# Kernel optimization log

Hardware: AMD Instinct MI355X
Metric: run time of the kernel (lower is better)

Reference implementation:

```python
import jax, jax.numpy as jnp
import numpy as np

B, L, D, HD, DC = 2, 2048, 2048, 64, 2048
NH = D // HD  # 32 heads


def _rms_norm(x, eps):
    return x * jax.lax.rsqrt(jnp.mean(jnp.square(x), axis=-1, keepdims=True) + eps)


def _apply_rope(x, rope):
    # x: [b,h,l,d]; rope: [2,l,d]. x_hat = interleave(-x_odd, x_even)
    x2 = x.reshape(*x.shape[:-1], HD // 2, 2)
    x_hat = jnp.stack([-x2[..., 1], x2[..., 0]], axis=-1).reshape(x.shape)
    return x * rope[0] + x_hat * rope[1]


def setup_inputs() -> dict:
    key = jax.random.key(0)
    ks = jax.random.split(key, 6)
    return {
        "x": jax.random.normal(ks[0], (B, L, D), jnp.float32),
        "condition": jax.random.normal(ks[1], (B, DC), jnp.float32),
        "rope": jax.random.normal(ks[2], (2, L, HD), jnp.float32),
        "w_ada": jax.random.normal(ks[3], (2 * D, DC), jnp.float32) * 0.02,
        "w_qkv": jax.random.normal(ks[4], (3 * D, D), jnp.float32) * 0.02,
        "w_out": jax.random.normal(ks[5], (D, D), jnp.float32) * 0.02,
        "qk_w": jnp.ones((HD,), jnp.float32),
    }


def reference(x, condition, rope, w_ada, w_qkv, w_out, qk_w):
    eps = jnp.finfo(x.dtype).eps
    # AdaRMSNorm
    ss = (condition @ w_ada.T)[:, None, :]          # [b,1,2D]
    shift, scale = jnp.split(ss, 2, axis=-1)
    h = _rms_norm(x, eps) * (1.0 + scale) + shift   # [b,l,D]
    # fused QKV projection: 'b l (n h d)'
    qkv = (h @ w_qkv.T).reshape(B, L, 3, NH, HD)
    qkv = jnp.transpose(qkv, (2, 0, 3, 1, 4))       # [3,b,h,l,d]
    q, k, v = qkv[0], qkv[1], qkv[2]
    # per-head RMSNorm (with affine weight) + RoPE
    q = _apply_rope(_rms_norm(q, eps) * qk_w, rope)
    k = _apply_rope(_rms_norm(k, eps) * qk_w, rope)
    # SDPA
    scores = jnp.einsum('bhqd,bhkd->bhqk', q, k) / jnp.sqrt(jnp.asarray(HD, x.dtype))
    attn = jax.nn.softmax(scores, axis=-1)
    o = jnp.einsum('bhqk,bhkd->bhqd', attn, v)      # [b,h,l,d]
    o = jnp.transpose(o, (0, 2, 1, 3)).reshape(B, L, D)
    return o @ w_out.T
```

## Files before the change

kernel.cpp:

```cpp
#include <hip/hip_runtime.h>


typedef __bf16 bf16x8 __attribute__((ext_vector_type(8)));
typedef float  f32x4  __attribute__((ext_vector_type(4)));
typedef float  f32x16 __attribute__((ext_vector_type(16)));

#define EPS_F32 1.1920929e-07f
#define QSCALE 0.18033688011112042f

#if defined(__has_builtin)
#  if __has_builtin(__builtin_amdgcn_exp2f)
#    define EXP2F(x) __builtin_amdgcn_exp2f(x)
#  else
#    define EXP2F(x) __expf((x) * 0.6931471805599453f)
#  endif
#  if __has_builtin(__builtin_amdgcn_rcpf)
#    define RCPF(x) __builtin_amdgcn_rcpf(x)
#  else
#    define RCPF(x) (1.0f / (x))
#  endif
#else
#  define EXP2F(x) __expf((x) * 0.6931471805599453f)
#  define RCPF(x) (1.0f / (x))
#endif

__device__ __forceinline__ float bf2f(unsigned int u16) {
  union { unsigned int i; float f; } v; v.i = (u16 & 0xffffu) << 16; return v.f;
}
__device__ __forceinline__ unsigned short f2bf(float f) {
  union { float f; unsigned int i; } v; v.f = f;
  unsigned int r = v.i + 0x7fffu + ((v.i >> 16) & 1u);
  return (unsigned short)(r >> 16);
}

__device__ __forceinline__ void gload16(const void* g, void* l) {
  __builtin_amdgcn_global_load_lds(
      (const __attribute__((address_space(1))) unsigned int*)(unsigned long long)g,
      (__attribute__((address_space(3))) unsigned int*)(unsigned int)(unsigned long long)l,
      16, 0, 0);
}

__global__ __launch_bounds__(256) void ada_gemm_kernel(
    const float* __restrict__ cond, const float* __restrict__ w_ada,
    float* __restrict__ ss)
{
  const int lane = threadIdx.x & 63;
  const int gw = blockIdx.x * 4 + (threadIdx.x >> 6);
  const int b = gw >> 12;
  const int j = gw & 4095;
  const float4* wr = (const float4*)(w_ada + j * 2048);
  const float4* cr = (const float4*)(cond + b * 2048);
  float acc = 0.f;
  #pragma unroll
  for (int k4 = 0; k4 < 8; ++k4) {
    float4 w = wr[lane + k4 * 64];
    float4 c = cr[lane + k4 * 64];
    acc += w.x * c.x + w.y * c.y + w.z * c.z + w.w * c.w;
  }
  #pragma unroll
  for (int off = 1; off < 64; off <<= 1) acc += __shfl_xor(acc, off);
  if (lane == 0) ss[b * 4096 + j] = acc;
}

__global__ __launch_bounds__(256) void ada_rms_kernel(
    const float* __restrict__ x, const float* __restrict__ ss,
    unsigned short* __restrict__ H)
{
  const int row = blockIdx.x;
  const int b = row >> 11;
  const int tid = threadIdx.x;
  const int lane = tid & 63, wave = tid >> 6;
  const float* xr = x + (size_t)row * 2048;
  float4 v0 = ((const float4*)xr)[tid * 2];
  float4 v1 = ((const float4*)xr)[tid * 2 + 1];
  float ssq = v0.x*v0.x + v0.y*v0.y + v0.z*v0.z + v0.w*v0.w
            + v1.x*v1.x + v1.y*v1.y + v1.z*v1.z + v1.w*v1.w;
  #pragma unroll
  for (int off = 1; off < 64; off <<= 1) ssq += __shfl_xor(ssq, off);
  __shared__ float red[4];
  if (lane == 0) red[wave] = ssq;
  __syncthreads();
  const float tot = red[0] + red[1] + red[2] + red[3];
  const float r = rsqrtf(tot * (1.f / 2048.f) + EPS_F32);
  const int c0 = tid * 8;
  const float* sh = ss + b * 4096;
  float xv[8] = {v0.x, v0.y, v0.z, v0.w, v1.x, v1.y, v1.z, v1.w};
  unsigned int pk[4];
  #pragma unroll
  for (int p = 0; p < 4; ++p) {
    const int c = c0 + p * 2;
    float h0 = xv[p*2+0] * r * (1.f + sh[2048 + c])     + sh[c];
    float h1 = xv[p*2+1] * r * (1.f + sh[2048 + c + 1]) + sh[c + 1];
    pk[p] = (unsigned int)f2bf(h0) | ((unsigned int)f2bf(h1) << 16);
  }
  *(uint4*)&H[(size_t)row * 2048 + c0] = make_uint4(pk[0], pk[1], pk[2], pk[3]);
}

__global__ __launch_bounds__(256) void cast_kernel(
    const float* __restrict__ src, unsigned short* __restrict__ dst, int n4)
{
  const int i = blockIdx.x * 256 + threadIdx.x;
  if (i >= n4) return;
  float4 v = ((const float4*)src)[i];
  unsigned int p0 = (unsigned int)f2bf(v.x) | ((unsigned int)f2bf(v.y) << 16);
  unsigned int p1 = (unsigned int)f2bf(v.z) | ((unsigned int)f2bf(v.w) << 16);
  *(uint2*)&dst[(size_t)i * 4] = make_uint2(p0, p1);
}

template <int MODE>
__global__ __launch_bounds__(256) void gemm_bt_kernel(
    const unsigned short* __restrict__ A,
    const unsigned short* __restrict__ Bw,
    void* __restrict__ Cv,
    unsigned short* __restrict__ vt,
    int M, int N, int K)
{
  __shared__ unsigned short As[128 * 32];
  __shared__ unsigned short Bs[128 * 32];
  const int tid  = threadIdx.x;
  const int lane = tid & 63;
  const int wave = tid >> 6;
  const int wm = (wave >> 1) * 64;
  const int wn = (wave & 1) * 64;
  const int bm = blockIdx.y * 128;
  const int bn = blockIdx.x * 128;

  f32x4 acc[4][4] = {};

  const int sm = tid >> 2;
  const int sk = (tid & 3) * 8;
  const unsigned short* Ap  = A  + (size_t)(bm + sm) * K + sk;
  const unsigned short* Ap2 = Ap + (size_t)64 * K;
  const unsigned short* Bp  = Bw + (size_t)(bn + sm) * K + sk;
  const unsigned short* Bp2 = Bp + (size_t)64 * K;
  unsigned short* lA  = &As[tid * 8];
  unsigned short* lA2 = &As[tid * 8 + 2048];
  unsigned short* lB  = &Bs[tid * 8];
  unsigned short* lB2 = &Bs[tid * 8 + 2048];

  const int fr = lane & 15;
  const int fk = (lane >> 4) * 8;

  for (int k0 = 0; k0 < K; k0 += 32) {
    __syncthreads();
    gload16(Ap  + k0, lA);
    gload16(Ap2 + k0, lA2);
    gload16(Bp  + k0, lB);
    gload16(Bp2 + k0, lB2);
    __syncthreads();

    bf16x8 af[4], bfr[4];
    #pragma unroll
    for (int i = 0; i < 4; ++i)
      af[i] = *(const bf16x8*)&As[(wm + i * 16 + fr) * 32 + fk];
    #pragma unroll
    for (int j = 0; j < 4; ++j)
      bfr[j] = *(const bf16x8*)&Bs[(wn + j * 16 + fr) * 32 + fk];
    #pragma unroll
    for (int i = 0; i < 4; ++i)
      #pragma unroll
      for (int j = 0; j < 4; ++j)
        acc[i][j] = __builtin_amdgcn_mfma_f32_16x16x32_bf16(af[i], bfr[j], acc[i][j], 0, 0, 0);
  }

  const int cr = (lane >> 4) * 4;
  const int cc = lane & 15;
  if (MODE == 2 && bn >= 4096) {
    #pragma unroll
    for (int i = 0; i < 4; ++i)
      #pragma unroll
      for (int j = 0; j < 4; ++j)
        #pragma unroll
        for (int r = 0; r < 4; ++r) {
          const int m  = bm + wm + i * 16 + cr + r;
          const int dg = bn + wn + j * 16 + cc - 4096;
          const int l  = m & 2047;
          const size_t dst = ((size_t)((m >> 11) * 32 + (dg >> 6)) * 64 + (dg & 63)) * 2048
                           + (l >> 6) * 64 + (l & 15) * 4 + ((l >> 4) & 3);
          vt[dst] = f2bf(acc[i][j][r]);
        }
  } else {
    #pragma unroll
    for (int i = 0; i < 4; ++i)
      #pragma unroll
      for (int j = 0; j < 4; ++j)
        #pragma unroll
        for (int r = 0; r < 4; ++r) {
          const int row = bm + wm + i * 16 + cr + r;
          const int col = bn + wn + j * 16 + cc;
          if (MODE != 0)
            ((unsigned short*)Cv)[(size_t)row * N + col] = f2bf(acc[i][j][r]);
          else
            ((float*)Cv)[(size_t)row * N + col] = acc[i][j][r];
        }
  }
}

__global__ __launch_bounds__(256) void qk_rope_kernel(
    unsigned short* __restrict__ QKV, const float* __restrict__ rope,
    const float* __restrict__ qk_w)
{
  const int lane = threadIdx.x & 63;
  const int gid = blockIdx.x * 4 + (threadIdx.x >> 6);
  const int l = gid & 2047;
  const int h = (gid >> 11) & 31;
  const int b = gid >> 16;
  const int base = (b * 2048 + l) * 6144 + h * 64 + lane;
  const float r0 = rope[l * 64 + lane];
  const float r1 = rope[131072 + l * 64 + lane];
  const float w  = qk_w[lane];
  #pragma unroll
  for (int t = 0; t < 2; ++t) {
    const int idx = base + 2048 * t;
    const float v = bf2f(QKV[idx]);
    float sq = v * v;
    #pragma unroll
    for (int off = 1; off < 64; off <<= 1) sq += __shfl_xor(sq, off);
    const float vn = v * rsqrtf(sq * (1.f / 64.f) + EPS_F32) * w;
    const float vp = __shfl_xor(vn, 1);
    const float vh = (lane & 1) ? vp : -vp;
    const float scale = (t == 0) ? QSCALE : 1.0f;
    QKV[idx] = f2bf((vn * r0 + vh * r1) * scale);
  }
}

__global__ __launch_bounds__(256) void attn_mfma_kernel(
    const unsigned short* __restrict__ QKV,
    const unsigned short* __restrict__ Vt,
    unsigned short* __restrict__ O)
{
  __shared__ unsigned short Ks[64 * 72];
  __shared__ unsigned short Vs[64 * 72];
  __shared__ unsigned short Ps[4 * 32 * 68];
  const int tid  = threadIdx.x;
  const int lane = tid & 63;
  const int wave = tid >> 6;
  const int qt = blockIdx.x;
  const int bh = blockIdx.y;
  const int b = bh >> 5, h = bh & 31;
  const int rowbase = b << 11;
  const int qbase = qt * 128 + wave * 32;

  const int m16  = lane & 15;
  const int quad = lane >> 4;
  const int m32  = lane & 31;
  const int hl   = lane >> 5;

  bf16x8 qf[2][2];
  #pragma unroll
  for (int qi = 0; qi < 2; ++qi)
    #pragma unroll
    for (int ch = 0; ch < 2; ++ch)
      qf[qi][ch] = *(const bf16x8*)&QKV[(size_t)(rowbase + qbase + qi * 16 + m16) * 6144
                                        + h * 64 + ch * 32 + quad * 8];

  const int sr = tid >> 2;
  const int sc = (tid & 3) * 16;
  const unsigned short* Kg = QKV + (size_t)(rowbase + sr) * 6144 + 2048 + h * 64 + sc;
  const unsigned short* Vg = Vt + (size_t)(bh * 64 + sr) * 2048 + sc;

  f32x16 accO[2] = {};
  float part[2][4] = {{0.f, 0.f, 0.f, 0.f}, {0.f, 0.f, 0.f, 0.f}};
  unsigned short* Pw = &Ps[(wave * 32) * 68];

  for (int kt = 0; kt < 32; ++kt) {
    __syncthreads();
    {
      const uint4* kp = (const uint4*)(Kg + (size_t)kt * 64 * 6144);
      const uint4* vp = (const uint4*)(Vg + kt * 64);
      uint4 k0 = kp[0], k1 = kp[1];
      uint4 v0 = vp[0], v1 = vp[1];
      *(uint4*)&Ks[sr * 72 + sc]     = k0;
      *(uint4*)&Ks[sr * 72 + sc + 8] = k1;
      *(uint4*)&Vs[sr * 72 + sc]     = v0;
      *(uint4*)&Vs[sr * 72 + sc + 8] = v1;
    }
    __syncthreads();

    unsigned int pk[2][4][2];
    #pragma unroll
    for (int kj = 0; kj < 4; ++kj) {
      bf16x8 kf0 = *(const bf16x8*)&Ks[(kj * 16 + m16) * 72 + quad * 8];
      bf16x8 kf1 = *(const bf16x8*)&Ks[(kj * 16 + m16) * 72 + 32 + quad * 8];
      #pragma unroll
      for (int qi = 0; qi < 2; ++qi) {
        f32x4 acc = {};
        acc = __builtin_amdgcn_mfma_f32_16x16x32_bf16(qf[qi][0], kf0, acc, 0, 0, 0);
        acc = __builtin_amdgcn_mfma_f32_16x16x32_bf16(qf[qi][1], kf1, acc, 0, 0, 0);
        #pragma unroll
        for (int r = 0; r < 4; ++r) {
          float p = EXP2F(acc[r]);
          part[qi][r] += p;
          unsigned int pb = f2bf(p);
          if (kj == 0)      pk[qi][r][0]  = pb;
          else if (kj == 1) pk[qi][r][0] |= pb << 16;
          else if (kj == 2) pk[qi][r][1]  = pb;
          else              pk[qi][r][1] |= pb << 16;
        }
      }
    }
    #pragma unroll
    for (int qi = 0; qi < 2; ++qi)
      #pragma unroll
      for (int r = 0; r < 4; ++r)
        *(uint2*)&Pw[(qi * 16 + quad * 4 + r) * 68 + m16 * 4] =
            make_uint2(pk[qi][r][0], pk[qi][r][1]);

    #pragma unroll
    for (int ch = 0; ch < 4; ++ch) {
      bf16x8 pa = *(const bf16x8*)&Pw[m32 * 68 + ch * 16 + hl * 8];
      #pragma unroll
      for (int dt = 0; dt < 2; ++dt) {
        bf16x8 vb = *(const bf16x8*)&Vs[(dt * 32 + m32) * 72 + ch * 16 + hl * 8];
        accO[dt] = __builtin_amdgcn_mfma_f32_32x32x16_bf16(pa, vb, accO[dt], 0, 0, 0);
      }
    }
  }

  #pragma unroll
  for (int qi = 0; qi < 2; ++qi)
    #pragma unroll
    for (int r = 0; r < 4; ++r)
      #pragma unroll
      for (int off = 1; off < 16; off <<= 1)
        part[qi][r] += __shfl_xor(part[qi][r], off);

  #pragma unroll
  for (int reg = 0; reg < 16; ++reg) {
    const int r  = reg & 3;
    const int qi = reg >> 3;
    const int qsrc = ((2 * (reg >> 2) + hl) & 3) * 16 + m16;
    const float rs = __shfl(part[qi][r], qsrc);
    const float inv = RCPF(rs);
    const int rho = (reg & 3) + 8 * (reg >> 2) + 4 * hl;
    const size_t base = (size_t)(rowbase + qbase + rho) * 2048 + h * 64;
    O[base + m32]      = f2bf(accO[0][reg] * inv);
    O[base + 32 + m32] = f2bf(accO[1][reg] * inv);
  }
}

extern "C" void kernel_launch(void* const* d_in, const int* in_sizes, int n_in,
                              void* d_out, int out_size, void* d_ws, size_t ws_size,
                              hipStream_t stream) {
  (void)in_sizes; (void)n_in; (void)out_size; (void)ws_size;
  const float* x     = (const float*)d_in[0];
  const float* cond  = (const float*)d_in[1];
  const float* rope  = (const float*)d_in[2];
  const float* w_ada = (const float*)d_in[3];
  const float* w_qkv = (const float*)d_in[4];
  const float* w_out = (const float*)d_in[5];
  const float* qk_w  = (const float*)d_in[6];
  float* out = (float*)d_out;

  char* ws = (char*)d_ws;
  float*          ss   = (float*)ws;
  unsigned short* H    = (unsigned short*)(ws + 32768);
  unsigned short* Wq   = H + 8388608;
  unsigned short* Wo   = Wq + 12582912;
  unsigned short* QKV  = Wo + 4194304;
  unsigned short* Vt_g = QKV + 25165824;

  ada_gemm_kernel<<<2048, 256, 0, stream>>>(cond, w_ada, ss);
  ada_rms_kernel<<<4096, 256, 0, stream>>>(x, ss, H);
  cast_kernel<<<12288, 256, 0, stream>>>(w_qkv, Wq, 3145728);
  cast_kernel<<<4096, 256, 0, stream>>>(w_out, Wo, 1048576);
  gemm_bt_kernel<2><<<dim3(48, 32), 256, 0, stream>>>(H, Wq, (void*)QKV, Vt_g, 4096, 6144, 2048);
  qk_rope_kernel<<<32768, 256, 0, stream>>>(QKV, rope, qk_w);
  attn_mfma_kernel<<<dim3(16, 64), 256, 0, stream>>>(QKV, Vt_g, H);
  gemm_bt_kernel<0><<<dim3(16, 32), 256, 0, stream>>>(H, Wo, (void*)out, nullptr, 4096, 2048, 2048);
}
```

Baseline: 502.2 us.

## Double attention query tile per wave, merge weight casts, cheaper P bf16 rounding

The attention kernel now gives each wave 64 query rows instead of 32, so a block covers 256 queries. Each K/V tile loaded into LDS is reused by twice as many queries, halving global K/V traffic and the barrier count per query. In exchange it uses more registers and LDS, runs half as many blocks (512) with a launch bound of 2 per SM, and orders blocks so the 64 heads share a query tile. It also merges the two weight-cast launches into one and switches the P-probability bf16 conversion to a cheaper round-half-up variant, which can change numerics slightly.

```diff
diff --git a/kernel.cpp b/kernel.cpp
--- a/kernel.cpp
+++ b/kernel.cpp
@@ -32,6 +32,10 @@
   unsigned int r = v.i + 0x7fffu + ((v.i >> 16) & 1u);
   return (unsigned short)(r >> 16);
 }
+__device__ __forceinline__ unsigned int f2bf_rn_u(float f) {
+  union { float f; unsigned int i; } v; v.f = f;
+  return v.i + 0x8000u;
+}
 
 __device__ __forceinline__ void gload16(const void* g, void* l) {
   __builtin_amdgcn_global_load_lds(
@@ -96,12 +100,14 @@
   *(uint4*)&H[(size_t)row * 2048 + c0] = make_uint4(pk[0], pk[1], pk[2], pk[3]);
 }
 
-__global__ __launch_bounds__(256) void cast_kernel(
-    const float* __restrict__ src, unsigned short* __restrict__ dst, int n4)
+__global__ __launch_bounds__(256) void cast2_kernel(
+    const float* __restrict__ a,
+    const float* __restrict__ b,
+    unsigned short* __restrict__ dst)
 {
   const int i = blockIdx.x * 256 + threadIdx.x;
-  if (i >= n4) return;
-  float4 v = ((const float4*)src)[i];
+  float4 v = (i < 3145728) ? ((const float4*)a)[i]
+                           : ((const float4*)b)[i - 3145728];
   unsigned int p0 = (unsigned int)f2bf(v.x) | ((unsigned int)f2bf(v.y) << 16);
   unsigned int p1 = (unsigned int)f2bf(v.z) | ((unsigned int)f2bf(v.w) << 16);
   *(uint2*)&dst[(size_t)i * 4] = make_uint2(p0, p1);
@@ -224,31 +230,32 @@
   }
 }
 
-__global__ __launch_bounds__(256) void attn_mfma_kernel(
+__global__ __launch_bounds__(256, 2) void attn_mfma_kernel(
     const unsigned short* __restrict__ QKV,
     const unsigned short* __restrict__ Vt,
     unsigned short* __restrict__ O)
 {
   __shared__ unsigned short Ks[64 * 72];
   __shared__ unsigned short Vs[64 * 72];
-  __shared__ unsigned short Ps[4 * 32 * 68];
+  __shared__ unsigned short Ps[4 * 64 * 68];
   const int tid  = threadIdx.x;
   const int lane = tid & 63;
   const int wave = tid >> 6;
-  const int qt = blockIdx.x;
-  const int bh = blockIdx.y;
+  const int blk = blockIdx.x;
+  const int bh = blk & 63;
+  const int qt = blk >> 6;
   const int b = bh >> 5, h = bh & 31;
   const int rowbase = b << 11;
-  const int qbase = qt * 128 + wave * 32;
+  const int qbase = qt * 256 + wave * 64;
 
   const int m16  = lane & 15;
   const int quad = lane >> 4;
   const int m32  = lane & 31;
   const int hl   = lane >> 5;
 
-  bf16x8 qf[2][2];
-  #pragma unroll
-  for (int qi = 0; qi < 2; ++qi)
+  bf16x8 qf[4][2];
+  #pragma unroll
+  for (int qi = 0; qi < 4; ++qi)
     #pragma unroll
     for (int ch = 0; ch < 2; ++ch)
       qf[qi][ch] = *(const bf16x8*)&QKV[(size_t)(rowbase + qbase + qi * 16 + m16) * 6144
@@ -259,9 +266,9 @@
   const unsigned short* Kg = QKV + (size_t)(rowbase + sr) * 6144 + 2048 + h * 64 + sc;
   const unsigned short* Vg = Vt + (size_t)(bh * 64 + sr) * 2048 + sc;
 
-  f32x16 accO[2] = {};
-  float part[2][4] = {{0.f, 0.f, 0.f, 0.f}, {0.f, 0.f, 0.f, 0.f}};
-  unsigned short* Pw = &Ps[(wave * 32) * 68];
+  f32x16 accO[2][2] = {};
+  float part[4][4] = {};
+  unsigned short* Pw = &Ps[(wave * 64) * 68];
 
   for (int kt = 0; kt < 32; ++kt) {
     __syncthreads();
@@ -277,13 +284,13 @@
     }
     __syncthreads();
 
-    unsigned int pk[2][4][2];
+    unsigned int pk[4][4][2];
     #pragma unroll
     for (int kj = 0; kj < 4; ++kj) {
       bf16x8 kf0 = *(const bf16x8*)&Ks[(kj * 16 + m16) * 72 + quad * 8];
       bf16x8 kf1 = *(const bf16x8*)&Ks[(kj * 16 + m16) * 72 + 32 + quad * 8];
       #pragma unroll
-      for (int qi = 0; qi < 2; ++qi) {
+      for (int qi = 0; qi < 4; ++qi) {
         f32x4 acc = {};
         acc = __builtin_amdgcn_mfma_f32_16x16x32_bf16(qf[qi][0], kf0, acc, 0, 0, 0);
         acc = __builtin_amdgcn_mfma_f32_16x16x32_bf16(qf[qi][1], kf1, acc, 0, 0, 0);
@@ -291,16 +298,16 @@
         for (int r = 0; r < 4; ++r) {
           float p = EXP2F(acc[r]);
           part[qi][r] += p;
-          unsigned int pb = f2bf(p);
-          if (kj == 0)      pk[qi][r][0]  = pb;
-          else if (kj == 1) pk[qi][r][0] |= pb << 16;
-          else if (kj == 2) pk[qi][r][1]  = pb;
-          else              pk[qi][r][1] |= pb << 16;
+          unsigned int pb = f2bf_rn_u(p);
+          if (kj == 0)      pk[qi][r][0]  = pb >> 16;
+          else if (kj == 1) pk[qi][r][0] |= pb & 0xffff0000u;
+          else if (kj == 2) pk[qi][r][1]  = pb >> 16;
+          else              pk[qi][r][1] |= pb & 0xffff0000u;
         }
       }
     }
     #pragma unroll
-    for (int qi = 0; qi < 2; ++qi)
+    for (int qi = 0; qi < 4; ++qi)
       #pragma unroll
       for (int r = 0; r < 4; ++r)
         *(uint2*)&Pw[(qi * 16 + quad * 4 + r) * 68 + m16 * 4] =
@@ -308,17 +315,19 @@
 
     #pragma unroll
     for (int ch = 0; ch < 4; ++ch) {
-      bf16x8 pa = *(const bf16x8*)&Pw[m32 * 68 + ch * 16 + hl * 8];
-      #pragma unroll
-      for (int dt = 0; dt < 2; ++dt) {
-        bf16x8 vb = *(const bf16x8*)&Vs[(dt * 32 + m32) * 72 + ch * 16 + hl * 8];
-        accO[dt] = __builtin_amdgcn_mfma_f32_32x32x16_bf16(pa, vb, accO[dt], 0, 0, 0);
-      }
+      bf16x8 pa0 = *(const bf16x8*)&Pw[m32 * 68 + ch * 16 + hl * 8];
+      bf16x8 pa1 = *(const bf16x8*)&Pw[(32 + m32) * 68 + ch * 16 + hl * 8];
+      bf16x8 vb0 = *(const bf16x8*)&Vs[m32 * 72 + ch * 16 + hl * 8];
+      bf16x8 vb1 = *(const bf16x8*)&Vs[(32 + m32) * 72 + ch * 16 + hl * 8];
+      accO[0][0] = __builtin_amdgcn_mfma_f32_32x32x16_bf16(pa0, vb0, accO[0][0], 0, 0, 0);
+      accO[0][1] = __builtin_amdgcn_mfma_f32_32x32x16_bf16(pa0, vb1, accO[0][1], 0, 0, 0);
+      accO[1][0] = __builtin_amdgcn_mfma_f32_32x32x16_bf16(pa1, vb0, accO[1][0], 0, 0, 0);
+      accO[1][1] = __builtin_amdgcn_mfma_f32_32x32x16_bf16(pa1, vb1, accO[1][1], 0, 0, 0);
     }
   }
 
   #pragma unroll
-  for (int qi = 0; qi < 2; ++qi)
+  for (int qi = 0; qi < 4; ++qi)
     #pragma unroll
     for (int r = 0; r < 4; ++r)
       #pragma unroll
@@ -326,16 +335,19 @@
         part[qi][r] += __shfl_xor(part[qi][r], off);
 
   #pragma unroll
-  for (int reg = 0; reg < 16; ++reg) {
-    const int r  = reg & 3;
-    const int qi = reg >> 3;
-    const int qsrc = ((2 * (reg >> 2) + hl) & 3) * 16 + m16;
-    const float rs = __shfl(part[qi][r], qsrc);
-    const float inv = RCPF(rs);
-    const int rho = (reg & 3) + 8 * (reg >> 2) + 4 * hl;
-    const size_t base = (size_t)(rowbase + qbase + rho) * 2048 + h * 64;
-    O[base + m32]      = f2bf(accO[0][reg] * inv);
-    O[base + 32 + m32] = f2bf(accO[1][reg] * inv);
+  for (int qs = 0; qs < 2; ++qs) {
+    #pragma unroll
+    for (int reg = 0; reg < 16; ++reg) {
+      const int r = reg & 3;
+      const int s = reg >> 2;
+      const int qsrc = ((2 * s + hl) & 3) * 16 + m16;
+      const float rs = __shfl(part[qs * 2 + (reg >> 3)][r], qsrc);
+      const float inv = RCPF(rs);
+      const int rho = r + 8 * s + 4 * hl;
+      const size_t base = (size_t)(rowbase + qbase + qs * 32 + rho) * 2048 + h * 64;
+      O[base + m32]      = f2bf(accO[qs][0][reg] * inv);
+      O[base + 32 + m32] = f2bf(accO[qs][1][reg] * inv);
+    }
   }
 }
 
@@ -362,10 +374,9 @@
 
   ada_gemm_kernel<<<2048, 256, 0, stream>>>(cond, w_ada, ss);
   ada_rms_kernel<<<4096, 256, 0, stream>>>(x, ss, H);
-  cast_kernel<<<12288, 256, 0, stream>>>(w_qkv, Wq, 3145728);
-  cast_kernel<<<4096, 256, 0, stream>>>(w_out, Wo, 1048576);
+  cast2_kernel<<<16384, 256, 0, stream>>>(w_qkv, w_out, Wq);
   gemm_bt_kernel<2><<<dim3(48, 32), 256, 0, stream>>>(H, Wq, (void*)QKV, Vt_g, 4096, 6144, 2048);
   qk_rope_kernel<<<32768, 256, 0, stream>>>(QKV, rope, qk_w);
-  attn_mfma_kernel<<<dim3(16, 64), 256, 0, stream>>>(QKV, Vt_g, H);
+  attn_mfma_kernel<<<512, 256, 0, stream>>>(QKV, Vt_g, H);
   gemm_bt_kernel<0><<<dim3(16, 32), 256, 0, stream>>>(H, Wo, (void*)out, nullptr, 4096, 2048, 2048);
 }
```

Result: faster. 477.8 us (-4.9%).
